# Kernel tuning notes

Hardware: AMD Instinct MI355X
Metric: run time of the kernel (lower is better)

## Reference

```python
import jax, jax.numpy as jnp
import numpy as np

B, T, I, H, FF, C = 4096, 512, 13, 7, 512, 1


def setup_inputs() -> dict:
    key = jax.random.key(0)
    ks = jax.random.split(key, 9)
    s_ih = 1.0 / np.sqrt(H)
    return {
        "x": jax.random.normal(ks[0], (B, T, I), dtype=jnp.float32),
        # PyTorch LSTM params, gate order i,f,g,o, uniform(-1/sqrt(H), 1/sqrt(H))
        "w_ih": jax.random.uniform(ks[1], (4 * H, I), minval=-s_ih, maxval=s_ih, dtype=jnp.float32),
        "w_hh": jax.random.uniform(ks[2], (4 * H, H), minval=-s_ih, maxval=s_ih, dtype=jnp.float32),
        "b_ih": jax.random.uniform(ks[3], (4 * H,), minval=-s_ih, maxval=s_ih, dtype=jnp.float32),
        "b_hh": jax.random.uniform(ks[4], (4 * H,), minval=-s_ih, maxval=s_ih, dtype=jnp.float32),
        "fc1_w": jax.random.uniform(ks[5], (FF, H), minval=-s_ih, maxval=s_ih, dtype=jnp.float32),
        "fc1_b": jax.random.uniform(ks[6], (FF,), minval=-s_ih, maxval=s_ih, dtype=jnp.float32),
        "fc_w": jax.random.uniform(ks[7], (C, FF), minval=-1.0 / np.sqrt(FF), maxval=1.0 / np.sqrt(FF), dtype=jnp.float32),
        "fc_b": jax.random.uniform(ks[8], (C,), minval=-1.0 / np.sqrt(FF), maxval=1.0 / np.sqrt(FF), dtype=jnp.float32),
    }


def _lstm_last_hidden(x, w_ih, w_hh, b_ih, b_hh):
    # Precompute input contributions for all timesteps: [B, T, 4H]
    xg = jnp.einsum("bti,gi->btg", x, w_ih) + b_ih

    def step(carry, xg_t):
        h, c = carry
        gates = xg_t + h @ w_hh.T + b_hh  # [B, 4H]
        i, f, g, o = jnp.split(gates, 4, axis=-1)
        i = jax.nn.sigmoid(i)
        f = jax.nn.sigmoid(f)
        g = jnp.tanh(g)
        o = jax.nn.sigmoid(o)
        c = f * c + i * g
        h = o * jnp.tanh(c)
        return (h, c), None

    h0 = jnp.zeros((x.shape[0], w_hh.shape[1]), dtype=x.dtype)
    (hn, _), _ = jax.lax.scan(step, (h0, h0), jnp.swapaxes(xg, 0, 1))
    return hn  # [B, H]


def reference(x, w_ih, w_hh, b_ih, b_hh, fc1_w, fc1_b, fc_w, fc_b):
    # Dropout(0.1) is identity in eval mode.
    hn = _lstm_last_hidden(x, w_ih, w_hh, b_ih, b_hh)
    out = jax.nn.relu(hn)
    out = jax.nn.relu(out @ fc1_w.T + fc1_b)
    return out @ fc_w.T + fc_b  # [B, 1]
```

## Files before the change

kernel.cpp:

```cpp
#include <hip/hip_runtime.h>

#define BB 4096
#define TN 512
#define IN 13
#define HN 7
#define FFD 512
#define CT 32
#define NCK (TN / CT)
#define GPB 2

#define SWZ(v, imm) __int_as_float(__builtin_amdgcn_ds_swizzle(__float_as_int(v), (imm)))
#define QB(v, q)    __int_as_float(__builtin_amdgcn_mov_dpp(__float_as_int(v), (q)*0x55, 0xF, 0xF, true))

__global__ __launch_bounds__(128, 4)
void lstm_fused(const float* __restrict__ x,
                const float* __restrict__ w_ih,
                const float* __restrict__ w_hh,
                const float* __restrict__ b_ih,
                const float* __restrict__ b_hh,
                const float* __restrict__ fc1_w,
                const float* __restrict__ fc1_b,
                const float* __restrict__ fc_w,
                const float* __restrict__ fc_b,
                float* __restrict__ out)
{
    __shared__ float xd[2][CT][64];
    __shared__ float xs[GPB][CT][16];

    const int tid  = threadIdx.x;
    const int wid  = tid >> 6;
    const int l64  = tid & 63;
    const int grp  = l64 >> 5;
    const int lane = l64 & 31;
    const int b    = blockIdx.x * GPB + grp;

    const int tau = lane & 3;
    const int ju  = lane >> 2;
    const int jj  = (ju < HN) ? ju : (HN - 1);
    const int row = tau * HN + jj;

    const float L2E = 1.4426950408889634f;

    float wih[IN];
    float bias = 0.0f;
    if (wid == 1) {
#pragma unroll
        for (int i = 0; i < IN; ++i) wih[i] = w_ih[row * IN + i];
        bias = b_ih[row] + b_hh[row];
    }

    auto produce = [&](int ck) {
        const float* src = x + ((long)b * TN + ck * CT + lane) * IN;
        float p[IN];
#pragma unroll
        for (int i = 0; i < IN; ++i) p[i] = src[i];
        float* dst = &xs[grp][lane][0];
        *(float4*)(dst)     = make_float4(p[0], p[1], p[2],  p[3]);
        *(float4*)(dst + 4) = make_float4(p[4], p[5], p[6],  p[7]);
        *(float4*)(dst + 8) = make_float4(p[8], p[9], p[10], p[11]);
        dst[12] = p[12];
        const int buf = ck & 1;
#pragma unroll
        for (int s = 0; s < CT; ++s) {
            const float* xr = &xs[grp][s][0];
            const float4 a  = *(const float4*)(xr);
            const float4 b4 = *(const float4*)(xr + 4);
            const float4 c4 = *(const float4*)(xr + 8);
            const float  d0 = xr[12];
            float s0 = fmaf(wih[0], a.x, bias);
            s0 = fmaf(wih[1], a.y, s0);
            s0 = fmaf(wih[2], a.z, s0);
            s0 = fmaf(wih[3], a.w, s0);
            float s1 = wih[4] * b4.x;
            s1 = fmaf(wih[5], b4.y, s1);
            s1 = fmaf(wih[6], b4.z, s1);
            s1 = fmaf(wih[7], b4.w, s1);
            float s2 = wih[8] * c4.x;
            s2 = fmaf(wih[9],  c4.y, s2);
            s2 = fmaf(wih[10], c4.z, s2);
            s2 = fmaf(wih[11], c4.w, s2);
            s2 = fmaf(wih[12], d0,   s2);
            xd[buf][s][l64] = (s0 + s1) + s2;
        }
    };

    float whh[HN];
    if (wid == 0) {
#pragma unroll
        for (int k = 0; k < HN; ++k) whh[k] = w_hh[row * HN + k];
    }
    const bool  is_tanh = (tau == 2);
    const float kmul = is_tanh ? (-2.0f * L2E) : (-L2E);
    const float sc   = is_tanh ?  2.0f : 1.0f;
    const float offc = is_tanh ? -1.0f : 0.0f;

    float h0 = 0.f, h1 = 0.f, h2 = 0.f, h3 = 0.f, h4 = 0.f, h5 = 0.f, h6 = 0.f;
    float cval = 0.0f;

    if (wid == 1) produce(0);
    __syncthreads();

    for (int ck = 0; ck < NCK; ++ck) {
        if (wid == 1) {
            if (ck + 1 < NCK) produce(ck + 1);
        } else {
            const int buf = ck & 1;
            float xr[CT];
#pragma unroll
            for (int s = 0; s < CT; ++s) xr[s] = xd[buf][s][l64];

#pragma unroll
            for (int s = 0; s < CT; ++s) {
                float s0 = fmaf(whh[0], h0, xr[s]);
                s0 = fmaf(whh[1], h1, s0);
                s0 = fmaf(whh[2], h2, s0);
                s0 = fmaf(whh[3], h3, s0);
                float s1 = whh[4] * h4;
                s1 = fmaf(whh[5], h5, s1);
                s1 = fmaf(whh[6], h6, s1);
                const float sg = s0 + s1;

                float e   = __builtin_amdgcn_exp2f(kmul * sg);
                float val = fmaf(__builtin_amdgcn_rcpf(1.0f + e), sc, offc);

                float iv = QB(val, 0);
                float fv = QB(val, 1);
                float gv = QB(val, 2);
                float ov = QB(val, 3);

                cval = fmaf(fv, cval, iv * gv);
                float e2 = __builtin_amdgcn_exp2f(-2.0f * L2E * cval);
                float th = fmaf(__builtin_amdgcn_rcpf(1.0f + e2), 2.0f, -1.0f);
                float hq = ov * th;

                h0 = SWZ(hq, (0  << 5));
                h1 = SWZ(hq, (4  << 5));
                h2 = SWZ(hq, (8  << 5));
                h3 = SWZ(hq, (12 << 5));
                h4 = SWZ(hq, (16 << 5));
                h5 = SWZ(hq, (20 << 5));
                h6 = SWZ(hq, (24 << 5));
            }
        }
        __syncthreads();
    }

    if (wid == 1) return;

    float hb[HN] = { fmaxf(h0,0.f), fmaxf(h1,0.f), fmaxf(h2,0.f), fmaxf(h3,0.f),
                     fmaxf(h4,0.f), fmaxf(h5,0.f), fmaxf(h6,0.f) };

    float acc = 0.0f;
#pragma unroll
    for (int k = 0; k < FFD / 32; ++k) {
        int r = lane + (k << 5);
        float s = fc1_b[r];
#pragma unroll
        for (int j = 0; j < HN; ++j) s = fmaf(fc1_w[r * HN + j], hb[j], s);
        s = fmaxf(s, 0.0f);
        acc = fmaf(fc_w[r], s, acc);
    }
#pragma unroll
    for (int o = 16; o >= 1; o >>= 1) acc += __shfl_xor(acc, o, 32);
    if (lane == 0) out[b] = acc + fc_b[0];
}

extern "C" void kernel_launch(void* const* d_in, const int* in_sizes, int n_in,
                              void* d_out, int out_size, void* d_ws, size_t ws_size,
                              hipStream_t stream) {
    const float* x     = (const float*)d_in[0];
    const float* w_ih  = (const float*)d_in[1];
    const float* w_hh  = (const float*)d_in[2];
    const float* b_ih  = (const float*)d_in[3];
    const float* b_hh  = (const float*)d_in[4];
    const float* fc1_w = (const float*)d_in[5];
    const float* fc1_b = (const float*)d_in[6];
    const float* fc_w  = (const float*)d_in[7];
    const float* fc_b  = (const float*)d_in[8];
    float* out = (float*)d_out;

    dim3 grid(BB / GPB);
    dim3 block(128);
    hipLaunchKernelGGL(lstm_fused, grid, block, 0, stream,
                       x, w_ih, w_hh, b_ih, b_hh, fc1_w, fc1_b, fc_w, fc_b, out);
}
```

Baseline: 96.90 us.

## Restructure LSTM producer warp with prefetch, packed FMA, and transposed staging

The producer wavefront now prefetches the next chunk of x into registers one chunk ahead and stores it to shared memory in a transposed layout. It computes the input projection with packed v_pk_fma_f32 over pairs of timesteps. The activation scale kmul is folded into the w_ih, w_hh and bias weights, which removes one multiply per step on the recurrent critical path. The consumer wave gets raised scheduling priority, the chunk size is halved, and launch bounds are raised for occupancy. The cost is more synchronisation rounds per sequence and higher register pressure from the prefetch buffer.

```diff
diff --git a/kernel.cpp b/kernel.cpp
--- a/kernel.cpp
+++ b/kernel.cpp
@@ -5,14 +5,20 @@
 #define IN 13
 #define HN 7
 #define FFD 512
-#define CT 32
+#define CT 16
 #define NCK (TN / CT)
 #define GPB 2
 
 #define SWZ(v, imm) __int_as_float(__builtin_amdgcn_ds_swizzle(__float_as_int(v), (imm)))
 #define QB(v, q)    __int_as_float(__builtin_amdgcn_mov_dpp(__float_as_int(v), (q)*0x55, 0xF, 0xF, true))
 
-__global__ __launch_bounds__(128, 4)
+__device__ __forceinline__ float2 pkfma(float2 a, float2 b, float2 c) {
+    float2 d;
+    asm("v_pk_fma_f32 %0, %1, %2, %3" : "=v"(d) : "v"(a), "v"(b), "v"(c));
+    return d;
+}
+
+__global__ __launch_bounds__(128, 7)
 void lstm_fused(const float* __restrict__ x,
                 const float* __restrict__ w_ih,
                 const float* __restrict__ w_hh,
@@ -24,8 +30,8 @@
                 const float* __restrict__ fc_b,
                 float* __restrict__ out)
 {
-    __shared__ float xd[2][CT][64];
-    __shared__ float xs[GPB][CT][16];
+    __shared__ float2 xd2[2][CT/2][64];
+    __shared__ float  xs[IN][GPB][CT];
 
     const int tid  = threadIdx.x;
     const int wid  = tid >> 6;
@@ -39,76 +45,103 @@
     const int jj  = (ju < HN) ? ju : (HN - 1);
     const int row = tau * HN + jj;
 
-    const float L2E = 1.4426950408889634f;
-
-    float wih[IN];
-    float bias = 0.0f;
-    if (wid == 1) {
-#pragma unroll
-        for (int i = 0; i < IN; ++i) wih[i] = w_ih[row * IN + i];
-        bias = b_ih[row] + b_hh[row];
-    }
-
-    auto produce = [&](int ck) {
-        const float* src = x + ((long)b * TN + ck * CT + lane) * IN;
-        float p[IN];
-#pragma unroll
-        for (int i = 0; i < IN; ++i) p[i] = src[i];
-        float* dst = &xs[grp][lane][0];
-        *(float4*)(dst)     = make_float4(p[0], p[1], p[2],  p[3]);
-        *(float4*)(dst + 4) = make_float4(p[4], p[5], p[6],  p[7]);
-        *(float4*)(dst + 8) = make_float4(p[8], p[9], p[10], p[11]);
-        dst[12] = p[12];
-        const int buf = ck & 1;
-#pragma unroll
-        for (int s = 0; s < CT; ++s) {
-            const float* xr = &xs[grp][s][0];
-            const float4 a  = *(const float4*)(xr);
-            const float4 b4 = *(const float4*)(xr + 4);
-            const float4 c4 = *(const float4*)(xr + 8);
-            const float  d0 = xr[12];
-            float s0 = fmaf(wih[0], a.x, bias);
-            s0 = fmaf(wih[1], a.y, s0);
-            s0 = fmaf(wih[2], a.z, s0);
-            s0 = fmaf(wih[3], a.w, s0);
-            float s1 = wih[4] * b4.x;
-            s1 = fmaf(wih[5], b4.y, s1);
-            s1 = fmaf(wih[6], b4.z, s1);
-            s1 = fmaf(wih[7], b4.w, s1);
-            float s2 = wih[8] * c4.x;
-            s2 = fmaf(wih[9],  c4.y, s2);
-            s2 = fmaf(wih[10], c4.z, s2);
-            s2 = fmaf(wih[11], c4.w, s2);
-            s2 = fmaf(wih[12], d0,   s2);
-            xd[buf][s][l64] = (s0 + s1) + s2;
-        }
-    };
-
-    float whh[HN];
-    if (wid == 0) {
-#pragma unroll
-        for (int k = 0; k < HN; ++k) whh[k] = w_hh[row * HN + k];
-    }
+    const float L2E  = 1.4426950408889634f;
     const bool  is_tanh = (tau == 2);
     const float kmul = is_tanh ? (-2.0f * L2E) : (-L2E);
     const float sc   = is_tanh ?  2.0f : 1.0f;
     const float offc = is_tanh ? -1.0f : 0.0f;
 
+    const int s_st = lane & 15;
+    const int h_st = (lane >> 4) & 1;
+    const int cb   = h_st * 7;
+    float2 w2[IN];
+    float2 bias2;
+    float  p[7];
+
+    float whh[HN];
+
+    if (wid == 1) {
+#pragma unroll
+        for (int i = 0; i < IN; ++i) {
+            const float w = kmul * w_ih[row * IN + i];
+            w2[i] = make_float2(w, w);
+        }
+        const float bsum = kmul * (b_ih[row] + b_hh[row]);
+        bias2 = make_float2(bsum, bsum);
+    } else {
+#pragma unroll
+        for (int k = 0; k < HN; ++k) whh[k] = kmul * w_hh[row * HN + k];
+        __builtin_amdgcn_s_setprio(1);
+    }
+
     float h0 = 0.f, h1 = 0.f, h2 = 0.f, h3 = 0.f, h4 = 0.f, h5 = 0.f, h6 = 0.f;
     float cval = 0.0f;
 
-    if (wid == 1) produce(0);
+    if (wid == 1) {
+        const float* src0 = x + ((long)b * TN + s_st) * IN + cb;
+#pragma unroll
+        for (int c = 0; c < 6; ++c) p[c] = src0[c];
+        if (h_st == 0) p[6] = src0[6];
+#pragma unroll
+        for (int c = 0; c < 6; ++c) xs[cb + c][grp][s_st] = p[c];
+        if (h_st == 0) xs[cb + 6][grp][s_st] = p[6];
+        {
+            const float* src1 = x + ((long)b * TN + CT + s_st) * IN + cb;
+#pragma unroll
+            for (int c = 0; c < 6; ++c) p[c] = src1[c];
+            if (h_st == 0) p[6] = src1[6];
+        }
+#pragma unroll
+        for (int q = 0; q < CT; q += 4) {
+            float2 accA = bias2, accB = bias2;
+#pragma unroll
+            for (int i = 0; i < IN; ++i) {
+                const float4 xv = *(const float4*)&xs[i][grp][q];
+                accA = pkfma(w2[i], make_float2(xv.x, xv.y), accA);
+                accB = pkfma(w2[i], make_float2(xv.z, xv.w), accB);
+            }
+            xd2[0][(q >> 1) + 0][l64] = accA;
+            xd2[0][(q >> 1) + 1][l64] = accB;
+        }
+    }
     __syncthreads();
 
     for (int ck = 0; ck < NCK; ++ck) {
         if (wid == 1) {
-            if (ck + 1 < NCK) produce(ck + 1);
+            const int nk = ck + 1;
+            if (nk < NCK) {
+#pragma unroll
+                for (int c = 0; c < 6; ++c) xs[cb + c][grp][s_st] = p[c];
+                if (h_st == 0) xs[cb + 6][grp][s_st] = p[6];
+                if (nk + 1 < NCK) {
+                    const float* src = x + ((long)b * TN + (nk + 1) * CT + s_st) * IN + cb;
+#pragma unroll
+                    for (int c = 0; c < 6; ++c) p[c] = src[c];
+                    if (h_st == 0) p[6] = src[6];
+                }
+                const int buf = nk & 1;
+#pragma unroll
+                for (int q = 0; q < CT; q += 4) {
+                    float2 accA = bias2, accB = bias2;
+#pragma unroll
+                    for (int i = 0; i < IN; ++i) {
+                        const float4 xv = *(const float4*)&xs[i][grp][q];
+                        accA = pkfma(w2[i], make_float2(xv.x, xv.y), accA);
+                        accB = pkfma(w2[i], make_float2(xv.z, xv.w), accB);
+                    }
+                    xd2[buf][(q >> 1) + 0][l64] = accA;
+                    xd2[buf][(q >> 1) + 1][l64] = accB;
+                }
+            }
         } else {
             const int buf = ck & 1;
             float xr[CT];
 #pragma unroll
-            for (int s = 0; s < CT; ++s) xr[s] = xd[buf][s][l64];
-
+            for (int pq = 0; pq < CT / 2; ++pq) {
+                const float2 v = xd2[buf][pq][l64];
+                xr[2 * pq]     = v.x;
+                xr[2 * pq + 1] = v.y;
+            }
 #pragma unroll
             for (int s = 0; s < CT; ++s) {
                 float s0 = fmaf(whh[0], h0, xr[s]);
@@ -120,18 +153,18 @@
                 s1 = fmaf(whh[6], h6, s1);
                 const float sg = s0 + s1;
 
-                float e   = __builtin_amdgcn_exp2f(kmul * sg);
+                float e   = __builtin_amdgcn_exp2f(sg);
                 float val = fmaf(__builtin_amdgcn_rcpf(1.0f + e), sc, offc);
 
-                float iv = QB(val, 0);
-                float fv = QB(val, 1);
-                float gv = QB(val, 2);
-                float ov = QB(val, 3);
+                const float iv = QB(val, 0);
+                const float fv = QB(val, 1);
+                const float gv = QB(val, 2);
+                const float ov = QB(val, 3);
 
                 cval = fmaf(fv, cval, iv * gv);
                 float e2 = __builtin_amdgcn_exp2f(-2.0f * L2E * cval);
                 float th = fmaf(__builtin_amdgcn_rcpf(1.0f + e2), 2.0f, -1.0f);
-                float hq = ov * th;
+                const float hq = ov * th;
 
                 h0 = SWZ(hq, (0  << 5));
                 h1 = SWZ(hq, (4  << 5));
@@ -153,7 +186,7 @@
     float acc = 0.0f;
 #pragma unroll
     for (int k = 0; k < FFD / 32; ++k) {
-        int r = lane + (k << 5);
+        const int r = lane + (k << 5);
         float s = fc1_b[r];
 #pragma unroll
         for (int j = 0; j < HN; ++j) s = fmaf(fc1_w[r * HN + j], hb[j], s);
```

Result: slower. 105.2 us (+8.6%).
